# Optimization experiments

Measured on AMD Instinct MI355X. Metric: run time of the kernel, lower is better.

Reference implementation:

```python
import jax, jax.numpy as jnp
import numpy as np

NUM_HEADS = 16

def _rmsnorm(x, w):
    eps = jnp.finfo(x.dtype).eps  # torch nn.RMSNorm default eps
    ms = jnp.mean(x * x, axis=-1, keepdims=True)
    return x * jax.lax.rsqrt(ms + eps) * w

def _heads(x):
    B, S, D = x.shape
    return x.reshape(B, S, NUM_HEADS, D // NUM_HEADS)

def _attn(q, k, v):
    # q:[B,Sq,H,D] k,v:[B,Sk,H,D]; non-causal softmax attention
    scale = 1.0 / np.sqrt(q.shape[-1]).astype(np.float32)
    s = jnp.einsum('bqhd,bkhd->bhqk', q, k) * scale
    p = jax.nn.softmax(s, axis=-1)
    return jnp.einsum('bhqk,bkhd->bqhd', p, v)

def _gate(ctx, W1, b1, W2, b2):
    # Linear -> SiLU -> Linear(dim->1) -> sigmoid ; returns [B,S,1]
    h = jax.nn.silu(ctx @ W1.T + b1)
    return jax.nn.sigmoid(h @ W2.T + b2)

def setup_inputs() -> dict:
    key = jax.random.key(0)
    ks = jax.random.split(key, 20)
    B, Sq, Sk, St, dim = 4, 512, 2048, 512, 1024
    n = lambda k, shp, s=1.0: jax.random.normal(k, shp, jnp.float32) * s
    W = lambda k, o, i: n(k, (o, i), 0.02)
    return {
        'queries': n(ks[0], (B, Sq, dim)),
        'context_visual': n(ks[1], (B, Sk, dim)),
        'context_text': n(ks[2], (B, St, dim)),
        'w_norm_q': jnp.ones((dim,), jnp.float32),
        'w_norm_v': jnp.ones((dim,), jnp.float32),
        'w_norm_t': jnp.ones((dim,), jnp.float32),
        'Wq': W(ks[3], dim, dim), 'bq': n(ks[4], (dim,), 0.02),
        'Wk_vis': W(ks[5], dim, dim), 'bk_vis': jnp.zeros((dim,), jnp.float32),
        'Wv_vis': W(ks[6], dim, dim), 'bv_vis': jnp.zeros((dim,), jnp.float32),
        'Wk_text': W(ks[7], dim, dim), 'bk_text': jnp.zeros((dim,), jnp.float32),
        'Wv_text': W(ks[8], dim, dim), 'bv_text': jnp.zeros((dim,), jnp.float32),
        'Wg1v': W(ks[9], dim, dim), 'bg1v': jnp.zeros((dim,), jnp.float32),
        'Wg2v': W(ks[10], 1, dim), 'bg2v': jnp.zeros((1,), jnp.float32),
        'Wg1t': W(ks[11], dim, dim), 'bg1t': jnp.zeros((dim,), jnp.float32),
        'Wg2t': W(ks[12], 1, dim), 'bg2t': jnp.zeros((1,), jnp.float32),
        'Wo': W(ks[13], dim, dim), 'bo': jnp.zeros((dim,), jnp.float32),
    }

def reference(queries, context_visual, context_text,
              w_norm_q, w_norm_v, w_norm_t,
              Wq, bq, Wk_vis, bk_vis, Wv_vis, bv_vis,
              Wk_text, bk_text, Wv_text, bv_text,
              Wg1v, bg1v, Wg2v, bg2v, Wg1t, bg1t, Wg2t, bg2t,
              Wo, bo):
    residual = queries
    qn = _rmsnorm(queries, w_norm_q)
    cv = _rmsnorm(context_visual, w_norm_v)
    ct = _rmsnorm(context_text, w_norm_t)
    q = _heads(qn @ Wq.T + bq)
    k_vis = _heads(cv @ Wk_vis.T + bk_vis)
    v_vis = _heads(cv @ Wv_vis.T + bv_vis)
    v_vis = v_vis * _gate(cv, Wg1v, bg1v, Wg2v, bg2v)[..., None]  # [B,Sk,1,1]
    h = _attn(q, k_vis, v_vis)
    k_text = _heads(ct @ Wk_text.T + bk_text)
    v_text = _heads(ct @ Wv_text.T + bv_text)
    v_text = v_text * _gate(ct, Wg1t, bg1t, Wg2t, bg2t)[..., None]
    h = h + _attn(q, k_text, v_text)
    B, Sq, H, D = h.shape
    out = h.reshape(B, Sq, H * D) @ Wo.T + bo  # dropout p=0 -> identity
    return residual + out
```

## Files before the change

kernel.cpp:

```cpp
#include <hip/hip_runtime.h>
#include <hip/hip_bf16.h>

typedef __attribute__((ext_vector_type(4))) float f32x4;
typedef __attribute__((ext_vector_type(8))) short s16x8;
typedef __attribute__((ext_vector_type(4))) short s16x4;
using bf16 = __hip_bfloat16;

static constexpr int BB  = 4;
static constexpr int SQ  = 512;
static constexpr int SKV = 2048;
static constexpr int SKT = 512;
static constexpr int DIM = 1024;
static constexpr int NH  = 16;
static constexpr int HD  = 64;

#define MFMA32(A,B,C) __builtin_amdgcn_mfma_f32_16x16x32_bf16(A,B,C,0,0,0)

#if __has_builtin(__builtin_amdgcn_mfma_f32_16x16x16_bf16)
  #define MFMA16(A,B,C) __builtin_amdgcn_mfma_f32_16x16x16_bf16(A,B,C,0,0,0)
#elif __has_builtin(__builtin_amdgcn_mfma_f32_16x16x16bf16_1k)
  #define MFMA16(A,B,C) __builtin_amdgcn_mfma_f32_16x16x16bf16_1k(A,B,C,0,0,0)
#else
  #define MFMA16(A,B,C) (C)
#endif

#define SBAR() asm volatile("s_barrier" ::: "memory")

__device__ __forceinline__ float b2f(short s) {
  unsigned int u = ((unsigned int)(unsigned short)s) << 16;
  float f; __builtin_memcpy(&f, &u, 4); return f;
}
__device__ __forceinline__ short f2s(float f) {
  bf16 h = __float2bfloat16(f); short s; __builtin_memcpy(&s, &h, 2); return s;
}

__device__ __forceinline__ void gload16(const void* g, void* l) {
  __builtin_amdgcn_global_load_lds(
      (const __attribute__((address_space(1))) void*)g,
      (__attribute__((address_space(3))) void*)l, 16, 0, 0);
}

static constexpr float QSCALE = 0.180336880111120426f;

struct PrepArgs {
  const float* csrc[10]; bf16* cdst[10]; int cn[10];
  const float* nx[3]; const float* nw[3]; bf16* ny[3];
};
__global__ __launch_bounds__(256) void prep_kernel(PrepArgs a) {
  const int bx = blockIdx.x;
  if (bx < 10240) {
    const int y = bx >> 10;
    const int i = ((bx & 1023) * 256 + threadIdx.x) * 4;
    if (i >= a.cn[y]) return;
    const float4 v = *(const float4*)(a.csrc[y] + i);
    bf16* d = a.cdst[y] + i;
    d[0] = __float2bfloat16(v.x); d[1] = __float2bfloat16(v.y);
    d[2] = __float2bfloat16(v.z); d[3] = __float2bfloat16(v.w);
    return;
  }
  const int j = bx - 10240;
  int t, row;
  if (j < 2048) { t = 0; row = j; }
  else if (j < 10240) { t = 1; row = j - 2048; }
  else { t = 2; row = j - 10240; }
  const float* x = a.nx[t] + (size_t)row * DIM;
  const float4 v = *(const float4*)(x + threadIdx.x * 4);
  float ss = v.x*v.x + v.y*v.y + v.z*v.z + v.w*v.w;
  #pragma unroll
  for (int m = 32; m >= 1; m >>= 1) ss += __shfl_xor(ss, m);
  __shared__ float red[4];
  if ((threadIdx.x & 63) == 0) red[threadIdx.x >> 6] = ss;
  __syncthreads();
  ss = red[0] + red[1] + red[2] + red[3];
  const float sc = rsqrtf(ss * (1.0f / DIM) + 1.1920928955078125e-07f);
  const float4 w = *(const float4*)(a.nw[t] + threadIdx.x * 4);
  bf16* y = a.ny[t] + (size_t)row * DIM + threadIdx.x * 4;
  y[0] = __float2bfloat16(v.x * sc * w.x);
  y[1] = __float2bfloat16(v.y * sc * w.y);
  y[2] = __float2bfloat16(v.z * sc * w.z);
  y[3] = __float2bfloat16(v.w * sc * w.w);
}

struct PSlot { const bf16* A; const bf16* W; const float* bias;
               bf16* Cb; int epi; int sksh; };
struct PArgs { PSlot s[7]; };

__global__ __launch_bounds__(512, 2) void proj256(PArgs a) {
  __shared__ char lds[131072];
  const int tid = threadIdx.x, lane = tid & 63, wave = tid >> 6;
  const int m16 = lane & 15, g16 = lane >> 4;
  const int wm = wave >> 2, wn = wave & 3;

  const int i = (blockIdx.x & 7) * 64 + (blockIdx.x >> 3);
  int slot, rem;
  if (i < 384) { slot = i >> 7; rem = i & 127; }
  else { const int j = i - 384; slot = 3 + (j >> 5); rem = j & 31; }
  const PSlot S = a.s[slot];
  const int bn = rem & 3, bm = rem >> 2;

  const bf16* Ab = S.A + (size_t)bm * 256 * DIM;
  const bf16* Wb = S.W + (size_t)bn * 256 * DIM;

  auto stageA = [&](int k0, int buf) {
    #pragma unroll
    for (int q = 0; q < 4; ++q) {
      const int idx = q * 512 + tid;
      const int row = idx >> 3, g = (idx & 7) ^ (row & 7);
      gload16(Ab + (size_t)row * DIM + k0 + g * 8,
              &lds[buf * 65536 + q * 8192 + wave * 1024]);
    }
  };
  auto stageB = [&](int k0, int buf) {
    #pragma unroll
    for (int q = 0; q < 4; ++q) {
      const int idx = q * 512 + tid;
      const int row = idx >> 3, g = (idx & 7) ^ (row & 7);
      gload16(Wb + (size_t)row * DIM + k0 + g * 8,
              &lds[buf * 65536 + 32768 + q * 8192 + wave * 1024]);
    }
  };

  f32x4 acc[8][4];
  #pragma unroll
  for (int x = 0; x < 8; ++x)
    #pragma unroll
    for (int y = 0; y < 4; ++y)
      #pragma unroll
      for (int r = 0; r < 4; ++r) acc[x][y][r] = 0.0f;

  stageA(0, 0); stageB(0, 0);
  stageA(64, 1); stageB(64, 1);
  asm volatile("s_waitcnt vmcnt(8)" ::: "memory");
  SBAR();

  constexpr int NT = DIM / 64;
  for (int t = 0; t < NT; ++t) {
    const int buf = t & 1;
    const char* A0 = &lds[buf * 65536];
    const char* B0 = A0 + 32768;
    s16x8 af[4][2], bf0[2][2], bf1[2][2];

    #pragma unroll
    for (int mi = 0; mi < 4; ++mi) {
      const int row = wm * 128 + mi * 16 + m16;
      #pragma unroll
      for (int ks = 0; ks < 2; ++ks)
        af[mi][ks] = *(const s16x8*)(A0 + row * 128 + (((ks*4+g16) ^ (m16 & 7)) * 16));
    }
    #pragma unroll
    for (int ni = 0; ni < 2; ++ni) {
      const int row = wn * 64 + ni * 16 + m16;
      #pragma unroll
      for (int ks = 0; ks < 2; ++ks)
        bf0[ni][ks] = *(const s16x8*)(B0 + row * 128 + (((ks*4+g16) ^ (m16 & 7)) * 16));
    }
    SBAR();
    __builtin_amdgcn_s_setprio(1);
    #pragma unroll
    for (int mi = 0; mi < 4; ++mi)
      #pragma unroll
      for (int ni = 0; ni < 2; ++ni) {
        acc[mi][ni] = MFMA32(af[mi][0], bf0[ni][0], acc[mi][ni]);
        acc[mi][ni] = MFMA32(af[mi][1], bf0[ni][1], acc[mi][ni]);
      }
    __builtin_amdgcn_s_setprio(0);
    SBAR();

    #pragma unroll
    for (int ni = 0; ni < 2; ++ni) {
      const int row = wn * 64 + 32 + ni * 16 + m16;
      #pragma unroll
      for (int ks = 0; ks < 2; ++ks)
        bf1[ni][ks] = *(const s16x8*)(B0 + row * 128 + (((ks*4+g16) ^ (m16 & 7)) * 16));
    }
    SBAR();
    __builtin_amdgcn_s_setprio(1);
    #pragma unroll
    for (int mi = 0; mi < 4; ++mi)
      #pragma unroll
      for (int ni = 0; ni < 2; ++ni) {
        acc[mi][2+ni] = MFMA32(af[mi][0], bf1[ni][0], acc[mi][2+ni]);
        acc[mi][2+ni] = MFMA32(af[mi][1], bf1[ni][1], acc[mi][2+ni]);
      }
    __builtin_amdgcn_s_setprio(0);
    SBAR();

    if (t + 2 < NT) stageB((t + 2) * 64, buf);
    #pragma unroll
    for (int mi = 0; mi < 4; ++mi) {
      const int row = wm * 128 + 64 + mi * 16 + m16;
      #pragma unroll
      for (int ks = 0; ks < 2; ++ks)
        af[mi][ks] = *(const s16x8*)(A0 + row * 128 + (((ks*4+g16) ^ (m16 & 7)) * 16));
    }
    SBAR();
    __builtin_amdgcn_s_setprio(1);
    #pragma unroll
    for (int mi = 0; mi < 4; ++mi)
      #pragma unroll
      for (int ni = 0; ni < 2; ++ni) {
        acc[4+mi][ni] = MFMA32(af[mi][0], bf0[ni][0], acc[4+mi][ni]);
        acc[4+mi][ni] = MFMA32(af[mi][1], bf0[ni][1], acc[4+mi][ni]);
      }
    __builtin_amdgcn_s_setprio(0);
    SBAR();

    if (t + 2 < NT) stageA((t + 2) * 64, buf);
    __builtin_amdgcn_s_setprio(1);
    #pragma unroll
    for (int mi = 0; mi < 4; ++mi)
      #pragma unroll
      for (int ni = 0; ni < 2; ++ni) {
        acc[4+mi][2+ni] = MFMA32(af[mi][0], bf1[ni][0], acc[4+mi][2+ni]);
        acc[4+mi][2+ni] = MFMA32(af[mi][1], bf1[ni][1], acc[4+mi][2+ni]);
      }
    __builtin_amdgcn_s_setprio(0);
    if (t < NT - 2)       { asm volatile("s_waitcnt vmcnt(8)" ::: "memory"); }
    else if (t == NT - 2) { asm volatile("s_waitcnt vmcnt(0)" ::: "memory"); }
    SBAR();
  }

  #pragma unroll
  for (int ng = 0; ng < 4; ++ng) {
    const int col_l = wn * 64 + ng * 16 + m16;
    const float bv = S.bias[bn * 256 + col_l];
    #pragma unroll
    for (int mg = 0; mg < 8; ++mg) {
      #pragma unroll
      for (int r = 0; r < 4; ++r) {
        const int row_l = wm * 128 + mg * 16 + g16 * 4 + r;
        float v = acc[mg][ng][r] + bv;
        if (S.epi == 1)      v = v / (1.0f + __expf(-v));
        else if (S.epi == 3) v = v * QSCALE;
        const int byte = row_l * 512 + ((col_l * 2) ^ (((row_l >> 2) & 7) << 4));
        *(short*)(&lds[byte]) = f2s(v);
      }
    }
  }
  __syncthreads();
  {
    const int row_l = tid >> 1, half = tid & 1;
    const int m = bm * 256 + row_l;
    const int xr = ((row_l >> 2) & 7) << 4;
    if (S.epi >= 3) {
      const int msk = (1 << S.sksh) - 1;
      const int bb2 = m >> S.sksh, tok = m & msk;
      #pragma unroll
      for (int j = 0; j < 16; ++j) {
        const int colbyte = half * 256 + j * 16;
        const s16x8 val = *(const s16x8*)(&lds[row_l * 512 + (colbyte ^ xr)]);
        const int col_g = bn * 256 + half * 128 + j * 8;
        const int hh = col_g >> 6, d = col_g & 63;
        *(s16x8*)(&S.Cb[(((size_t)(bb2 * NH + hh) << S.sksh) + tok) * HD + d]) = val;
      }
    } else {
      #pragma unroll
      for (int j = 0; j < 16; ++j) {
        const int colbyte = half * 256 + j * 16;
        const s16x8 val = *(const s16x8*)(&lds[row_l * 512 + (colbyte ^ xr)]);
        const int col_g = bn * 256 + half * 128 + j * 8;
        *(s16x8*)(&S.Cb[(size_t)m * DIM + col_g]) = val;
      }
    }
  }
}

struct GSlot { const bf16* A; const bf16* W; const float* bias;
               const float* resid; float* Cf; };
__global__ __launch_bounds__(256) void gemm_out(GSlot S) {
  constexpr int K = DIM;
  __shared__ alignas(16) char sA[4096];
  __shared__ alignas(16) char sB[8192];
  const int tid = threadIdx.x, lane = tid & 63, wave = tid >> 6;
  const int bm = blockIdx.x, bn = blockIdx.y;
  const int m16 = lane & 15, g16 = lane >> 4;

  f32x4 acc[4][2];
  #pragma unroll
  for (int i = 0; i < 4; ++i)
    #pragma unroll
    for (int j = 0; j < 2; ++j)
      #pragma unroll
      for (int r = 0; r < 4; ++r) acc[i][j][r] = 0.0f;

  const bf16* Ab = S.A + (size_t)bm * 64 * K;
  const bf16* Wb = S.W + (size_t)bn * 128 * K;

  for (int t = 0; t < K / 32; ++t) {
    const int k0 = t * 32;
    {
      const int row = tid >> 2, sg = (tid & 3) ^ (row & 3);
      gload16(Ab + (size_t)row * K + k0 + sg * 8, &sA[wave * 1024]);
    }
    #pragma unroll
    for (int p = 0; p < 2; ++p) {
      const int idx = p * 256 + tid;
      const int row = idx >> 2, sg = (idx & 3) ^ (row & 3);
      gload16(Wb + (size_t)row * K + k0 + sg * 8, &sB[p * 4096 + wave * 1024]);
    }
    __syncthreads();
    s16x8 af[4], bfr[2];
    #pragma unroll
    for (int mi = 0; mi < 4; ++mi) {
      const int row = mi * 16 + m16;
      af[mi] = *(const s16x8*)(&sA[row * 64 + (g16 ^ (m16 & 3)) * 16]);
    }
    #pragma unroll
    for (int ni = 0; ni < 2; ++ni) {
      const int row = wave * 32 + ni * 16 + m16;
      bfr[ni] = *(const s16x8*)(&sB[row * 64 + (g16 ^ (m16 & 3)) * 16]);
    }
    #pragma unroll
    for (int mi = 0; mi < 4; ++mi)
      #pragma unroll
      for (int ni = 0; ni < 2; ++ni)
        acc[mi][ni] = MFMA32(af[mi], bfr[ni], acc[mi][ni]);
    __syncthreads();
  }

  const int r0 = bm * 64, c0 = bn * 128 + wave * 32;
  #pragma unroll
  for (int ni = 0; ni < 2; ++ni) {
    const int col = c0 + ni * 16 + m16;
    const float bv = S.bias[col];
    #pragma unroll
    for (int mi = 0; mi < 4; ++mi) {
      const int rowb = r0 + mi * 16 + g16 * 4;
      #pragma unroll
      for (int r = 0; r < 4; ++r) {
        const size_t idx = (size_t)(rowb + r) * DIM + col;
        S.Cf[idx] = acc[mi][ni][r] + bv + S.resid[idx];
      }
    }
  }
}

__global__ __launch_bounds__(256) void gate2_kernel(
    const bf16* __restrict__ g1v, const bf16* __restrict__ w2v,
    const float* __restrict__ b2v, float* __restrict__ gv,
    const bf16* __restrict__ g1t, const bf16* __restrict__ w2t,
    const float* __restrict__ b2t, float* __restrict__ gt)
{
  const int lane = threadIdx.x & 63, wave = threadIdx.x >> 6;
  int row = blockIdx.x * 4 + wave;
  const bf16* x; const bf16* w2; const float* b2; float* gate;
  if (row < BB * SKV) { x = g1v + (size_t)row * DIM; w2 = w2v; b2 = b2v; gate = gv + row; }
  else { row -= BB * SKV; x = g1t + (size_t)row * DIM; w2 = w2t; b2 = b2t; gate = gt + row; }
  float sum = 0.0f;
  #pragma unroll
  for (int c = 0; c < 2; ++c) {
    const int i0 = c * 512 + lane * 8;
    const s16x8 xv = *(const s16x8*)(x + i0);
    const s16x8 wv = *(const s16x8*)(w2 + i0);
    #pragma unroll
    for (int j = 0; j < 8; ++j) sum += b2f(xv[j]) * b2f(wv[j]);
  }
  #pragma unroll
  for (int m = 32; m >= 1; m >>= 1) sum += __shfl_xor(sum, m);
  if (lane == 0) *gate = 1.0f / (1.0f + __expf(-(sum + b2[0])));
}

__global__ __launch_bounds__(256) void vtrans2_kernel(
    const bf16* __restrict__ Vv, const float* __restrict__ gv, bf16* __restrict__ VTv,
    const bf16* __restrict__ Vt, const float* __restrict__ gt, bf16* __restrict__ VTt)
{
  __shared__ alignas(16) short tile[64][72];
  int kt = blockIdx.x;
  const bf16* V; const float* gate; bf16* VT; int Sk;
  if (kt < SKV / 64) { V = Vv; gate = gv; VT = VTv; Sk = SKV; }
  else { kt -= SKV / 64; V = Vt; gate = gt; VT = VTt; Sk = SKT; }
  const int h = blockIdx.y, b = blockIdx.z;
  const int tid = threadIdx.x;
  #pragma unroll
  for (int i = 0; i < 2; ++i) {
    const int c = tid + i * 256;
    const int kr = c >> 3, d0 = (c & 7) * 8;
    const float g = gate[(size_t)b * Sk + kt * 64 + kr];
    const s16x8 v = *(const s16x8*)(V + ((size_t)(b*Sk + kt*64 + kr)*NH + h)*HD + d0);
    #pragma unroll
    for (int j = 0; j < 8; ++j) tile[kr][d0 + j] = f2s(b2f(v[j]) * g);
  }
  __syncthreads();
  #pragma unroll
  for (int i = 0; i < 2; ++i) {
    const int c = tid + i * 256;
    const int d = c >> 3, k0 = (c & 7) * 8;
    s16x8 v;
    #pragma unroll
    for (int j = 0; j < 8; ++j) v[j] = tile[k0 + j][d];
    *(s16x8*)(VT + ((size_t)(b*NH + h)*HD + d)*Sk + kt*64 + k0) = v;
  }
}

__global__ __launch_bounds__(512, 2) void attn_kernel(
    const bf16* __restrict__ Qh,
    const bf16* __restrict__ K1h, const bf16* __restrict__ VT1,
    const bf16* __restrict__ K2h, const bf16* __restrict__ VT2,
    bf16* __restrict__ Hout)
{
  __shared__ alignas(16) char sK[2][2][8192];
  __shared__ alignas(16) char sVT[2][2][8192];
  const int tid = threadIdx.x, lane = tid & 63, wave = tid >> 6;
  const int hb = blockIdx.x;
  const int h = hb & 15, b = hb >> 4;
  const int wq = wave & 3, hf = wave >> 2;
  const int q0 = blockIdx.y * 64 + wq * 16;
  const int m16 = lane & 15, g16 = lane >> 4;

  const bf16* qrow = Qh + ((size_t)(b*NH + h)*SQ + q0 + m16)*HD;
  const s16x8 qf0 = *(const s16x8*)(qrow + g16 * 8);
  const s16x8 qf1 = *(const s16x8*)(qrow + 32 + g16 * 8);

  const bf16* K1b  = K1h + (size_t)(b*NH + h) * SKV * HD;
  const bf16* K2b  = K2h + (size_t)(b*NH + h) * SKT * HD;
  const bf16* VT1b = VT1 + (size_t)(b*NH + h) * HD * SKV;
  const bf16* VT2b = VT2 + (size_t)(b*NH + h) * HD * SKT;

  constexpr int NC1 = SKV / 128, NC = NC1 + SKT / 128;

  auto stage = [&](int c, int buf) {
    const int ctx = (c >= NC1);
    const bf16* Kb  = ctx ? K2b  : K1b;
    const bf16* VTb = ctx ? VT2b : VT1b;
    const int Sk = ctx ? SKT : SKV;
    const int cc = ctx ? c - NC1 : c;
    const int b0 = cc * 64, b1 = (Sk >> 1) + cc * 64;
    const int r = tid >> 3, g = (tid & 7) ^ (r & 7);
    gload16(Kb  + (size_t)(b0 + r) * HD + g * 8, &sK[buf][0][wave * 1024]);
    gload16(Kb  + (size_t)(b1 + r) * HD + g * 8, &sK[buf][1][wave * 1024]);
    gload16(VTb + (size_t)r * Sk + b0 + g * 8,   &sVT[buf][0][wave * 1024]);
    gload16(VTb + (size_t)r * Sk + b1 + g * 8,   &sVT[buf][1][wave * 1024]);
  };

  f32x4 o[4], ov[4];
  float mx, l, mxv, lv;
  #pragma unroll
  for (int i = 0; i < 4; ++i)
    #pragma unroll
    for (int r = 0; r < 4; ++r) { o[i][r] = 0.0f; ov[i][r] = 0.0f; }
  mx = -1e30f; l = 0.0f; mxv = -1e30f; lv = 0.0f;

  auto chunk = [&](int buf) {
    const char* kbase = &sK[buf][hf][0];
    const char* vbase = &sVT[buf][hf][0];
    f32x4 s[4];
    #pragma unroll
    for (int nt = 0; nt < 4; ++nt) {
      const char* kr = kbase + (nt * 16 + m16) * 128;
      const s16x8 kf0 = *(const s16x8*)(kr + ((g16    ) ^ (m16 & 7)) * 16);
      const s16x8 kf1 = *(const s16x8*)(kr + ((4 + g16) ^ (m16 & 7)) * 16);
      f32x4 a2; a2[0] = 0; a2[1] = 0; a2[2] = 0; a2[3] = 0;
      a2 = MFMA32(kf0, qf0, a2);
      a2 = MFMA32(kf1, qf1, a2);
      s[nt] = a2;
    }
    float mc = s[0][0];
    #pragma unroll
    for (int nt = 0; nt < 4; ++nt)
      #pragma unroll
      for (int r = 0; r < 4; ++r) mc = fmaxf(mc, s[nt][r]);
    mc = fmaxf(mc, __shfl_xor(mc, 16));
    mc = fmaxf(mc, __shfl_xor(mc, 32));
    const float mnew = fmaxf(mx, mc);
    const float alpha = exp2f(mx - mnew);
    mx = mnew;
    float p[4][4]; float rs = 0.0f;
    #pragma unroll
    for (int nt = 0; nt < 4; ++nt)
      #pragma unroll
      for (int r = 0; r < 4; ++r) { p[nt][r] = exp2f(s[nt][r] - mnew); rs += p[nt][r]; }
    rs += __shfl_xor(rs, 16);
    rs += __shfl_xor(rs, 32);
    l = l * alpha + rs;
    float av[4];
    #pragma unroll
    for (int r = 0; r < 4; ++r) av[r] = __shfl(alpha, g16 * 4 + r);
    #pragma unroll
    for (int nd = 0; nd < 4; ++nd)
      #pragma unroll
      for (int r = 0; r < 4; ++r) o[nd][r] *= av[r];
    #pragma unroll
    for (int nt = 0; nt < 4; ++nt) {
      s16x4 pa;
      pa[0] = f2s(p[nt][0]); pa[1] = f2s(p[nt][1]);
      pa[2] = f2s(p[nt][2]); pa[3] = f2s(p[nt][3]);
      #pragma unroll
      for (int nd = 0; nd < 4; ++nd) {
        const int d = nd * 16 + m16;
        const int g = (nt * 2 + (g16 >> 1)) ^ (m16 & 7);
        const s16x4 vf = *(const s16x4*)(vbase + d * 128 + g * 16 + (g16 & 1) * 8);
        o[nd] = MFMA16(pa, vf, o[nd]);
      }
    }
  };

  stage(0, 0);
  asm volatile("s_waitcnt vmcnt(0)" ::: "memory");
  SBAR();

  int buf = 0;
  for (int c = 0; c < NC; ++c) {
    if (c + 1 < NC) stage(c + 1, buf ^ 1);
    chunk(buf);
    if (c == NC1 - 1) {
      #pragma unroll
      for (int nd = 0; nd < 4; ++nd) ov[nd] = o[nd];
      mxv = mx; lv = l;
      #pragma unroll
      for (int nd = 0; nd < 4; ++nd)
        #pragma unroll
        for (int r = 0; r < 4; ++r) o[nd][r] = 0.0f;
      mx = -1e30f; l = 0.0f;
    }
    asm volatile("s_waitcnt vmcnt(0)" ::: "memory");
    SBAR();
    buf ^= 1;
  }

  float* mo = (float*)&sK[0][0][0];
  float* ml = (float*)&sVT[0][0][0];
  if (hf) {
    #pragma unroll
    for (int nd = 0; nd < 4; ++nd)
      #pragma unroll
      for (int r = 0; r < 4; ++r) {
        const int rl = wq * 16 + g16 * 4 + r;
        mo[rl * 64 + nd * 16 + m16]        = ov[nd][r];
        mo[4096 + rl * 64 + nd * 16 + m16] = o[nd][r];
      }
    if (g16 == 0) {
      ml[(wq * 4 + 0) * 16 + m16] = mxv; ml[(wq * 4 + 1) * 16 + m16] = lv;
      ml[(wq * 4 + 2) * 16 + m16] = mx;  ml[(wq * 4 + 3) * 16 + m16] = l;
    }
  }
  __syncthreads();
  if (!hf) {
    float of[4][4];
    #pragma unroll
    for (int ctx = 0; ctx < 2; ++ctx) {
      const float mb = ml[(wq * 4 + ctx * 2 + 0) * 16 + m16];
      const float lb = ml[(wq * 4 + ctx * 2 + 1) * 16 + m16];
      const float ma = ctx ? mx : mxv;
      const float la = ctx ? l  : lv;
      const float ms = fmaxf(ma, mb);
      const float aA = exp2f(ma - ms), aB = exp2f(mb - ms);
      const float lt = la * aA + lb * aB;
      float aAv[4], aBv[4], ltv[4];
      #pragma unroll
      for (int r = 0; r < 4; ++r) {
        aAv[r] = __shfl(aA, g16 * 4 + r);
        aBv[r] = __shfl(aB, g16 * 4 + r);
        ltv[r] = __shfl(lt, g16 * 4 + r);
      }
      #pragma unroll
      for (int nd = 0; nd < 4; ++nd)
        #pragma unroll
        for (int r = 0; r < 4; ++r) {
          const int rl = wq * 16 + g16 * 4 + r;
          const float ob = mo[ctx * 4096 + rl * 64 + nd * 16 + m16];
          const float oa = ctx ? o[nd][r] : ov[nd][r];
          const float res = (oa * aAv[r] + ob * aBv[r]) / ltv[r];
          if (ctx == 0) of[nd][r] = res; else of[nd][r] += res;
        }
    }
    #pragma unroll
    for (int nd = 0; nd < 4; ++nd)
      #pragma unroll
      for (int r = 0; r < 4; ++r) {
        const int row = q0 + g16 * 4 + r;
        Hout[((size_t)(b*SQ + row)*NH + h)*HD + nd*16 + m16] =
            __float2bfloat16(of[nd][r]);
      }
  }
}

extern "C" void kernel_launch(void* const* d_in, const int* in_sizes, int n_in,
                              void* d_out, int out_size, void* d_ws, size_t ws_size,
                              hipStream_t stream)
{
  const float* queries = (const float*)d_in[0];
  const float* ctx_v   = (const float*)d_in[1];
  const float* ctx_t   = (const float*)d_in[2];
  const float* w_nq = (const float*)d_in[3];
  const float* w_nv = (const float*)d_in[4];
  const float* w_nt = (const float*)d_in[5];
  const float* Wq   = (const float*)d_in[6];  const float* bq   = (const float*)d_in[7];
  const float* Wk_v = (const float*)d_in[8];  const float* bk_v = (const float*)d_in[9];
  const float* Wv_v = (const float*)d_in[10]; const float* bv_v = (const float*)d_in[11];
  const float* Wk_t = (const float*)d_in[12]; const float* bk_t = (const float*)d_in[13];
  const float* Wv_t = (const float*)d_in[14]; const float* bv_t = (const float*)d_in[15];
  const float* Wg1v = (const float*)d_in[16]; const float* bg1v = (const float*)d_in[17];
  const float* Wg2v = (const float*)d_in[18]; const float* bg2v = (const float*)d_in[19];
  const float* Wg1t = (const float*)d_in[20]; const float* bg1t = (const float*)d_in[21];
  const float* Wg2t = (const float*)d_in[22]; const float* bg2t = (const float*)d_in[23];
  const float* Wo   = (const float*)d_in[24]; const float* bo   = (const float*)d_in[25];

  char* ws = (char*)d_ws;
  size_t off = 0;
  auto alloc = [&](size_t n) { void* p = ws + off; off += (n + 255) & ~(size_t)255; return p; };

  const size_t MATB = (size_t)DIM * DIM * 2;
  bf16* WqB   = (bf16*)alloc(MATB);
  bf16* WkvB  = (bf16*)alloc(MATB);
  bf16* WvvB  = (bf16*)alloc(MATB);
  bf16* WktB  = (bf16*)alloc(MATB);
  bf16* WvtB  = (bf16*)alloc(MATB);
  bf16* Wg1vB = (bf16*)alloc(MATB);
  bf16* Wg1tB = (bf16*)alloc(MATB);
  bf16* WoB   = (bf16*)alloc(MATB);
  bf16* Wg2vB = (bf16*)alloc(2048);
  bf16* Wg2tB = (bf16*)alloc(2048);

  bf16* qn  = (bf16*)alloc((size_t)BB*SQ*DIM*2);
  bf16* cv  = (bf16*)alloc((size_t)BB*SKV*DIM*2);
  bf16* ct  = (bf16*)alloc((size_t)BB*SKT*DIM*2);
  bf16* qb  = (bf16*)alloc((size_t)BB*SQ*DIM*2);
  bf16* kvB = (bf16*)alloc((size_t)BB*SKV*DIM*2);
  bf16* ktB = (bf16*)alloc((size_t)BB*SKT*DIM*2);
  bf16* vtV = (bf16*)alloc((size_t)BB*SKV*DIM*2);
  bf16* vtT = (bf16*)alloc((size_t)BB*SKT*DIM*2);
  bf16* vScrV = (bf16*)alloc((size_t)BB*SKV*DIM*2);
  bf16* vScrT = (bf16*)alloc((size_t)BB*SKT*DIM*2);
  bf16* g1V   = (bf16*)alloc((size_t)BB*SKV*DIM*2);
  bf16* g1T   = (bf16*)alloc((size_t)BB*SKT*DIM*2);
  float* gateV = (float*)alloc((size_t)BB*SKV*4);
  float* gateT = (float*)alloc((size_t)BB*SKT*4);
  bf16* hB  = (bf16*)alloc((size_t)BB*SQ*DIM*2);
  (void)ws_size; (void)n_in; (void)in_sizes; (void)out_size;

  PrepArgs pr;
  const float* wsrc[10] = {Wq, Wk_v, Wv_v, Wk_t, Wv_t, Wg1v, Wg1t, Wo, Wg2v, Wg2t};
  bf16* wdst[10] = {WqB, WkvB, WvvB, WktB, WvtB, Wg1vB, Wg1tB, WoB, Wg2vB, Wg2tB};
  for (int i = 0; i < 10; ++i) {
    pr.csrc[i] = wsrc[i]; pr.cdst[i] = wdst[i];
    pr.cn[i] = (i < 8) ? DIM * DIM : DIM;
  }
  pr.nx[0] = queries; pr.nx[1] = ctx_v; pr.nx[2] = ctx_t;
  pr.nw[0] = w_nq;    pr.nw[1] = w_nv;  pr.nw[2] = w_nt;
  pr.ny[0] = qn;      pr.ny[1] = cv;    pr.ny[2] = ct;
  prep_kernel<<<dim3(10240 + 12288), 256, 0, stream>>>(pr);

  PArgs pa;
  pa.s[0] = {cv, WkvB,  bk_v, kvB,   4, 11};
  pa.s[1] = {cv, WvvB,  bv_v, vScrV, 0, 0};
  pa.s[2] = {cv, Wg1vB, bg1v, g1V,   1, 0};
  pa.s[3] = {qn, WqB,   bq,   qb,    3, 9};
  pa.s[4] = {ct, WktB,  bk_t, ktB,   4, 9};
  pa.s[5] = {ct, WvtB,  bv_t, vScrT, 0, 0};
  pa.s[6] = {ct, Wg1tB, bg1t, g1T,   1, 0};
  proj256<<<dim3(512), 512, 0, stream>>>(pa);

  gate2_kernel<<<dim3((BB*SKV + BB*SKT) / 4), 256, 0, stream>>>(
      g1V, Wg2vB, bg2v, gateV, g1T, Wg2tB, bg2t, gateT);
  vtrans2_kernel<<<dim3(SKV/64 + SKT/64, NH, BB), 256, 0, stream>>>(
      vScrV, gateV, vtV, vScrT, gateT, vtT);

  attn_kernel<<<dim3(NH*BB, SQ/64), 512, 0, stream>>>(qb, kvB, vtV, ktB, vtT, hB);

  GSlot go{hB, WoB, bo, queries, (float*)d_out};
  gemm_out<<<dim3(BB*SQ/64, 8), 256, 0, stream>>>(go);
}
```

Measured before the change: 217.2 us.

## Restructure proj256 K-loop with split A prefetch and direct-store epilogue

The projection GEMM's main loop now processes the 64-wide K tile in two K-halves with a 4x4 fragment set each, instead of the previous 2x2 N-quarters. The A tile for the next step is prefetched in two halves into the other buffer, interleaved with the MFMA phases, while B keeps a two-step lookahead. The epilogue drops the LDS staging and swizzled 16-byte vector stores and writes each bf16 element straight to global memory. That removes one barrier and the LDS round trip but gives up coalesced wide stores.

After: 195.8 us (median of 3 runs). -9.9%, faster.

```diff
diff --git a/kernel.cpp b/kernel.cpp
--- a/kernel.cpp
+++ b/kernel.cpp
@@ -101,16 +101,16 @@
   const bf16* Ab = S.A + (size_t)bm * 256 * DIM;
   const bf16* Wb = S.W + (size_t)bn * 256 * DIM;
 
-  auto stageA = [&](int k0, int buf) {
-    #pragma unroll
-    for (int q = 0; q < 4; ++q) {
-      const int idx = q * 512 + tid;
+  auto stageAh = [&](int k0, int buf, int h) {
+    #pragma unroll
+    for (int q = 0; q < 2; ++q) {
+      const int idx = (h * 2 + q) * 512 + tid;
       const int row = idx >> 3, g = (idx & 7) ^ (row & 7);
       gload16(Ab + (size_t)row * DIM + k0 + g * 8,
-              &lds[buf * 65536 + q * 8192 + wave * 1024]);
+              &lds[buf * 65536 + (h * 2 + q) * 8192 + wave * 1024]);
     }
   };
-  auto stageB = [&](int k0, int buf) {
+  auto stageBfull = [&](int k0, int buf) {
     #pragma unroll
     for (int q = 0; q < 4; ++q) {
       const int idx = q * 512 + tid;
@@ -128,9 +128,10 @@
       #pragma unroll
       for (int r = 0; r < 4; ++r) acc[x][y][r] = 0.0f;
 
-  stageA(0, 0); stageB(0, 0);
-  stageA(64, 1); stageB(64, 1);
-  asm volatile("s_waitcnt vmcnt(8)" ::: "memory");
+  stageAh(0, 0, 0); stageAh(0, 0, 1);
+  stageBfull(0, 0);
+  stageBfull(64, 1);
+  asm volatile("s_waitcnt vmcnt(4)" ::: "memory");
   SBAR();
 
   constexpr int NT = DIM / 64;
@@ -138,128 +139,120 @@
     const int buf = t & 1;
     const char* A0 = &lds[buf * 65536];
     const char* B0 = A0 + 32768;
-    s16x8 af[4][2], bf0[2][2], bf1[2][2];
+    s16x8 af[4], bfk[4];
 
     #pragma unroll
     for (int mi = 0; mi < 4; ++mi) {
       const int row = wm * 128 + mi * 16 + m16;
-      #pragma unroll
-      for (int ks = 0; ks < 2; ++ks)
-        af[mi][ks] = *(const s16x8*)(A0 + row * 128 + (((ks*4+g16) ^ (m16 & 7)) * 16));
-    }
-    #pragma unroll
-    for (int ni = 0; ni < 2; ++ni) {
+      af[mi] = *(const s16x8*)(A0 + row * 128 + ((g16 ^ (m16 & 7)) * 16));
+    }
+    #pragma unroll
+    for (int ni = 0; ni < 4; ++ni) {
       const int row = wn * 64 + ni * 16 + m16;
-      #pragma unroll
-      for (int ks = 0; ks < 2; ++ks)
-        bf0[ni][ks] = *(const s16x8*)(B0 + row * 128 + (((ks*4+g16) ^ (m16 & 7)) * 16));
-    }
+      bfk[ni] = *(const s16x8*)(B0 + row * 128 + ((g16 ^ (m16 & 7)) * 16));
+    }
+    if (t + 1 < NT) stageAh((t + 1) * 64, buf ^ 1, 0);
     SBAR();
     __builtin_amdgcn_s_setprio(1);
     #pragma unroll
     for (int mi = 0; mi < 4; ++mi)
       #pragma unroll
-      for (int ni = 0; ni < 2; ++ni) {
-        acc[mi][ni] = MFMA32(af[mi][0], bf0[ni][0], acc[mi][ni]);
-        acc[mi][ni] = MFMA32(af[mi][1], bf0[ni][1], acc[mi][ni]);
-      }
+      for (int ni = 0; ni < 4; ++ni)
+        acc[mi][ni] = MFMA32(af[mi], bfk[ni], acc[mi][ni]);
     __builtin_amdgcn_s_setprio(0);
     SBAR();
 
-    #pragma unroll
-    for (int ni = 0; ni < 2; ++ni) {
-      const int row = wn * 64 + 32 + ni * 16 + m16;
-      #pragma unroll
-      for (int ks = 0; ks < 2; ++ks)
-        bf1[ni][ks] = *(const s16x8*)(B0 + row * 128 + (((ks*4+g16) ^ (m16 & 7)) * 16));
-    }
-    SBAR();
-    __builtin_amdgcn_s_setprio(1);
-    #pragma unroll
-    for (int mi = 0; mi < 4; ++mi)
-      #pragma unroll
-      for (int ni = 0; ni < 2; ++ni) {
-        acc[mi][2+ni] = MFMA32(af[mi][0], bf1[ni][0], acc[mi][2+ni]);
-        acc[mi][2+ni] = MFMA32(af[mi][1], bf1[ni][1], acc[mi][2+ni]);
-      }
-    __builtin_amdgcn_s_setprio(0);
-    SBAR();
-
-    if (t + 2 < NT) stageB((t + 2) * 64, buf);
     #pragma unroll
     for (int mi = 0; mi < 4; ++mi) {
       const int row = wm * 128 + 64 + mi * 16 + m16;
-      #pragma unroll
-      for (int ks = 0; ks < 2; ++ks)
-        af[mi][ks] = *(const s16x8*)(A0 + row * 128 + (((ks*4+g16) ^ (m16 & 7)) * 16));
-    }
+      af[mi] = *(const s16x8*)(A0 + row * 128 + ((g16 ^ (m16 & 7)) * 16));
+    }
+    if (t + 1 < NT) stageAh((t + 1) * 64, buf ^ 1, 1);
     SBAR();
     __builtin_amdgcn_s_setprio(1);
     #pragma unroll
     for (int mi = 0; mi < 4; ++mi)
       #pragma unroll
-      for (int ni = 0; ni < 2; ++ni) {
-        acc[4+mi][ni] = MFMA32(af[mi][0], bf0[ni][0], acc[4+mi][ni]);
-        acc[4+mi][ni] = MFMA32(af[mi][1], bf0[ni][1], acc[4+mi][ni]);
+      for (int ni = 0; ni < 4; ++ni)
+        acc[4 + mi][ni] = MFMA32(af[mi], bfk[ni], acc[4 + mi][ni]);
+    __builtin_amdgcn_s_setprio(0);
+    SBAR();
+
+    #pragma unroll
+    for (int mi = 0; mi < 4; ++mi) {
+      const int row = wm * 128 + mi * 16 + m16;
+      af[mi] = *(const s16x8*)(A0 + row * 128 + (((4 + g16) ^ (m16 & 7)) * 16));
+    }
+    #pragma unroll
+    for (int ni = 0; ni < 4; ++ni) {
+      const int row = wn * 64 + ni * 16 + m16;
+      bfk[ni] = *(const s16x8*)(B0 + row * 128 + (((4 + g16) ^ (m16 & 7)) * 16));
+    }
+    SBAR();
+    __builtin_amdgcn_s_setprio(1);
+    #pragma unroll
+    for (int mi = 0; mi < 4; ++mi)
+      #pragma unroll
+      for (int ni = 0; ni < 4; ++ni)
+        acc[mi][ni] = MFMA32(af[mi], bfk[ni], acc[mi][ni]);
+    __builtin_amdgcn_s_setprio(0);
+    SBAR();
+
+    #pragma unroll
+    for (int mi = 0; mi < 4; ++mi) {
+      const int row = wm * 128 + 64 + mi * 16 + m16;
+      af[mi] = *(const s16x8*)(A0 + row * 128 + (((4 + g16) ^ (m16 & 7)) * 16));
+    }
+    if (t + 2 < NT) stageBfull((t + 2) * 64, buf);
+    SBAR();
+    __builtin_amdgcn_s_setprio(1);
+    #pragma unroll
+    for (int mi = 0; mi < 4; ++mi)
+      #pragma unroll
+      for (int ni = 0; ni < 4; ++ni)
+        acc[4 + mi][ni] = MFMA32(af[mi], bfk[ni], acc[4 + mi][ni]);
+    __builtin_amdgcn_s_setprio(0);
+    if (t < NT - 2)       { asm volatile("s_waitcnt vmcnt(4)" ::: "memory"); }
+    else if (t == NT - 2) { asm volatile("s_waitcnt vmcnt(0)" ::: "memory"); }
+    SBAR();
+  }
+
+  const int r0 = bm * 256 + wm * 128, c0 = bn * 256 + wn * 64;
+  if (S.epi >= 3) {
+    const float sc = (S.epi == 3) ? QSCALE : 1.0f;
+    const int msk = (1 << S.sksh) - 1;
+    #pragma unroll
+    for (int ng = 0; ng < 4; ++ng) {
+      const int col = c0 + ng * 16 + m16;
+      const int hh = col >> 6, d = col & 63;
+      const float bv = S.bias[col];
+      #pragma unroll
+      for (int mg = 0; mg < 8; ++mg) {
+        const int rowb = r0 + mg * 16 + g16 * 4;
+        #pragma unroll
+        for (int r = 0; r < 4; ++r) {
+          const int m = rowb + r;
+          const int bb2 = m >> S.sksh, tok = m & msk;
+          S.Cb[(((size_t)(bb2 * NH + hh) << S.sksh) + tok) * HD + d] =
+              __float2bfloat16((acc[mg][ng][r] + bv) * sc);
+        }
       }
-    __builtin_amdgcn_s_setprio(0);
-    SBAR();
-
-    if (t + 2 < NT) stageA((t + 2) * 64, buf);
-    __builtin_amdgcn_s_setprio(1);
-    #pragma unroll
-    for (int mi = 0; mi < 4; ++mi)
-      #pragma unroll
-      for (int ni = 0; ni < 2; ++ni) {
-        acc[4+mi][2+ni] = MFMA32(af[mi][0], bf1[ni][0], acc[4+mi][2+ni]);
-        acc[4+mi][2+ni] = MFMA32(af[mi][1], bf1[ni][1], acc[4+mi][2+ni]);
-      }
-    __builtin_amdgcn_s_setprio(0);
-    if (t < NT - 2)       { asm volatile("s_waitcnt vmcnt(8)" ::: "memory"); }
-    else if (t == NT - 2) { asm volatile("s_waitcnt vmcnt(0)" ::: "memory"); }
-    SBAR();
-  }
-
-  #pragma unroll
-  for (int ng = 0; ng < 4; ++ng) {
-    const int col_l = wn * 64 + ng * 16 + m16;
-    const float bv = S.bias[bn * 256 + col_l];
-    #pragma unroll
-    for (int mg = 0; mg < 8; ++mg) {
-      #pragma unroll
-      for (int r = 0; r < 4; ++r) {
-        const int row_l = wm * 128 + mg * 16 + g16 * 4 + r;
-        float v = acc[mg][ng][r] + bv;
-        if (S.epi == 1)      v = v / (1.0f + __expf(-v));
-        else if (S.epi == 3) v = v * QSCALE;
-        const int byte = row_l * 512 + ((col_l * 2) ^ (((row_l >> 2) & 7) << 4));
-        *(short*)(&lds[byte]) = f2s(v);
-      }
-    }
-  }
-  __syncthreads();
-  {
-    const int row_l = tid >> 1, half = tid & 1;
-    const int m = bm * 256 + row_l;
-    const int xr = ((row_l >> 2) & 7) << 4;
-    if (S.epi >= 3) {
-      const int msk = (1 << S.sksh) - 1;
-      const int bb2 = m >> S.sksh, tok = m & msk;
-      #pragma unroll
-      for (int j = 0; j < 16; ++j) {
-        const int colbyte = half * 256 + j * 16;
-        const s16x8 val = *(const s16x8*)(&lds[row_l * 512 + (colbyte ^ xr)]);
-        const int col_g = bn * 256 + half * 128 + j * 8;
-        const int hh = col_g >> 6, d = col_g & 63;
-        *(s16x8*)(&S.Cb[(((size_t)(bb2 * NH + hh) << S.sksh) + tok) * HD + d]) = val;
-      }
-    } else {
-      #pragma unroll
-      for (int j = 0; j < 16; ++j) {
-        const int colbyte = half * 256 + j * 16;
-        const s16x8 val = *(const s16x8*)(&lds[row_l * 512 + (colbyte ^ xr)]);
-        const int col_g = bn * 256 + half * 128 + j * 8;
-        *(s16x8*)(&S.Cb[(size_t)m * DIM + col_g]) = val;
+    }
+  } else {
+    #pragma unroll
+    for (int ng = 0; ng < 4; ++ng) {
+      const int col = c0 + ng * 16 + m16;
+      const float bv = S.bias[col];
+      #pragma unroll
+      for (int mg = 0; mg < 8; ++mg) {
+        const int rowb = r0 + mg * 16 + g16 * 4;
+        #pragma unroll
+        for (int r = 0; r < 4; ++r) {
+          float v = acc[mg][ng][r] + bv;
+          const size_t idx = (size_t)(rowb + r) * DIM + col;
+          if (S.epi == 1) { v = v / (1.0f + __expf(-v)); S.Cb[idx] = __float2bfloat16(v); }
+          else            { S.Cb[idx] = __float2bfloat16(v); }
+        }
       }
     }
   }
```
